# Kernel optimization log

Hardware: AMD Instinct MI355X
Metric: run time of the kernel (lower is better)

## Reference

```python
import jax, jax.numpy as jnp
import numpy as np

N_NODES = 100000
N_EDGES = 1600000
D_IN = 128
D_MSG = 128
D_HID = 128
D_EDGE = 5
D_CAT = D_IN + D_MSG  # 256
D_U1, D_U2, D_OUT = 214, 172, 128  # delta = (256-128)//3 = 42


def _leaky(x):
    return jax.nn.leaky_relu(x, negative_slope=0.01)


def setup_inputs() -> dict:
    key = jax.random.key(0)
    ks = jax.random.split(key, 12)
    def kaiming(k, shape):
        fan_in = shape[1]
        gain = np.sqrt(2.0 / (1.0 + 0.01 ** 2))
        return jax.random.normal(k, shape, dtype=jnp.float32) * (gain / np.sqrt(fan_in))
    x = jax.random.normal(ks[0], (N_NODES, D_IN), dtype=jnp.float32)
    edge_index = jax.random.randint(ks[1], (2, N_EDGES), 0, N_NODES, dtype=jnp.int64)
    edge_attr = jax.random.normal(ks[2], (N_EDGES, D_EDGE), dtype=jnp.float32)
    return {
        "x": x, "edge_index": edge_index, "edge_attr": edge_attr,
        "Wm1": kaiming(ks[3], (D_HID, D_EDGE)), "bm1": jnp.zeros((D_HID,), jnp.float32),
        "Wm2": kaiming(ks[4], (D_HID, D_HID)), "bm2": jnp.zeros((D_HID,), jnp.float32),
        "Wm3": kaiming(ks[5], (D_MSG, D_HID)), "bm3": jnp.zeros((D_MSG,), jnp.float32),
        "ln_g": jnp.ones((D_CAT,), jnp.float32), "ln_b": jnp.zeros((D_CAT,), jnp.float32),
        "Wu1": kaiming(ks[6], (D_U1, D_CAT)), "bu1": jnp.zeros((D_U1,), jnp.float32),
        "Wu2": kaiming(ks[7], (D_U2, D_U1)), "bu2": jnp.zeros((D_U2,), jnp.float32),
        "Wu3": kaiming(ks[8], (D_OUT, D_U2)), "bu3": jnp.zeros((D_OUT,), jnp.float32),
    }


def reference(x, edge_index, edge_attr, Wm1, bm1, Wm2, bm2, Wm3, bm3,
              ln_g, ln_b, Wu1, bu1, Wu2, bu2, Wu3, bu3):
    # --- message: MLP2 on edge_attr only ---  [E, D_MSG]
    h = _leaky(edge_attr @ Wm1.T + bm1)
    h = _leaky(h @ Wm2.T + bm2)
    msg = h @ Wm3.T + bm3
    # --- aggregate: scatter-add per destination node (edge_index[1]) ---
    dst = edge_index[1]
    aggr = jax.ops.segment_sum(msg, dst, num_segments=x.shape[0])  # [N, D_MSG]
    # --- update: LayerNorm(concat) then shrinking MLP ---
    cat = jnp.concatenate([x, aggr], axis=-1)  # [N, 256]
    mu = jnp.mean(cat, axis=-1, keepdims=True)
    var = jnp.mean((cat - mu) ** 2, axis=-1, keepdims=True)
    nrm = (cat - mu) * jax.lax.rsqrt(var + 1e-5) * ln_g + ln_b
    u = _leaky(nrm @ Wu1.T + bu1)
    u = _leaky(u @ Wu2.T + bu2)
    return u @ Wu3.T + bu3  # [N, D_OUT]
```

## Files before the change

### kernel.cpp

```cpp
#include <hip/hip_runtime.h>

#define N_NODES 100000
#define N_EDGES 1600000
#define STRN 264
#define NBLK_SCAN 391

#define MSG_SCALE 4096.0f
#define MSG_INV   0.000244140625f

typedef __attribute__((ext_vector_type(4))) float floatx4;
typedef __attribute__((ext_vector_type(8))) __bf16 bf16x8;
typedef __attribute__((ext_vector_type(8))) unsigned short ushort8;
typedef __attribute__((ext_vector_type(4))) unsigned short ushort4v;

#define WS_AGGR   0ull
#define WS_COUNTS 51200000ull
#define WS_OFFS   51600384ull
#define WS_PART   52000768ull
#define WS_DSTS   52002816ull
#define WS_ATTRS  58402816ull
#define WS_W2     90402816ull
#define WS_W3     (WS_W2 + 32768ull)
#define WS_WU1    (WS_W3 + 32768ull)
#define WS_WU2    (WS_WU1 + 114688ull)
#define WS_WU3    (WS_WU2 + 86016ull)
#define WS_W1     (WS_WU3 + 49152ull)

__device__ __forceinline__ unsigned short tobf(float f) {
  return __builtin_bit_cast(unsigned short, (__bf16)f);
}

__device__ __forceinline__ float leaky(float v) { return fmaxf(v, 0.01f * v); }

__device__ __forceinline__ int swz(int row, int ch) {
  return row * 128 + (ch ^ ((row & 7) << 3));
}

__device__ __forceinline__ int msw(int e, int ch) {
  return e * 16 + (ch ^ (((e >> 1) & 3) << 2));
}

__device__ __forceinline__ int dsw(int e) { return e + ((e >> 5) << 3); }

__global__ void prep_kernel(const float* __restrict__ Wm1, const float* __restrict__ Wm2,
                            const float* __restrict__ Wm3,
                            const float* __restrict__ Wu1, const float* __restrict__ Wu2,
                            const float* __restrict__ Wu3,
                            unsigned short* __restrict__ o1b,
                            unsigned short* __restrict__ o2, unsigned short* __restrict__ o3,
                            unsigned short* __restrict__ o1p, unsigned short* __restrict__ o2p,
                            unsigned short* __restrict__ o3p) {
  int i = blockIdx.x * 256 + threadIdx.x;
  if (i < 16384) {
    o2[i] = tobf(Wm2[i]);
  } else if (i < 32768) {
    int j = i - 16384; o3[j] = tobf(Wm3[j]);
  } else if (i < 32768 + 57344) {
    int j = i - 32768; int n = j >> 8, k = j & 255;
    o1p[j] = (n < 214) ? tobf(Wu1[n * 256 + k]) : (unsigned short)0;
  } else if (i < 90112 + 43008) {
    int j = i - 90112; int n = j / 224, k = j - n * 224;
    o2p[j] = (n < 172 && k < 214) ? tobf(Wu2[n * 214 + k]) : (unsigned short)0;
  } else if (i < 133120 + 24576) {
    int j = i - 133120; int n = j / 192, k = j - n * 192;
    o3p[j] = (k < 172) ? tobf(Wu3[n * 172 + k]) : (unsigned short)0;
  } else if (i < 157696 + 4096) {
    int j = i - 157696; int n = j >> 5, k = j & 31;
    o1b[j] = (k < 5) ? tobf(Wm1[n * 5 + k]) : (unsigned short)0;
  }
}

__global__ void hist_kernel(const int* __restrict__ dst, int* __restrict__ counts,
                            int* __restrict__ rank) {
  int e = blockIdx.x * 256 + threadIdx.x;
  if (e < N_EDGES) rank[e] = atomicAdd(&counts[dst[e]], 1);
}

__global__ void scanA_kernel(const int* __restrict__ counts, int* __restrict__ offs,
                             int* __restrict__ partials) {
  __shared__ int tmp[256];
  const int t = threadIdx.x;
  const int i = blockIdx.x * 256 + t;
  int v = (i < N_NODES) ? counts[i] : 0;
  tmp[t] = v;
  __syncthreads();
  for (int off = 1; off < 256; off <<= 1) {
    int a = (t >= off) ? tmp[t - off] : 0;
    __syncthreads();
    tmp[t] += a;
    __syncthreads();
  }
  if (i < N_NODES) offs[i] = tmp[t] - v;
  if (t == 255) partials[blockIdx.x] = tmp[255];
}

__global__ void scanB_kernel(int* __restrict__ partials) {
  __shared__ int tmp[512];
  const int t = threadIdx.x;
  int v = (t < NBLK_SCAN) ? partials[t] : 0;
  tmp[t] = v;
  __syncthreads();
  for (int off = 1; off < 512; off <<= 1) {
    int a = (t >= off) ? tmp[t - off] : 0;
    __syncthreads();
    tmp[t] += a;
    __syncthreads();
  }
  if (t < NBLK_SCAN) partials[t] = tmp[t] - v;
}

__global__ void scatter_kernel(const int* __restrict__ dst, const int* __restrict__ offs,
                               const int* __restrict__ parts, const int* __restrict__ rank,
                               const float* __restrict__ attr,
                               float* __restrict__ attrS, int* __restrict__ dsts) {
  int e = blockIdx.x * 256 + threadIdx.x;
  if (e < N_EDGES) {
    int d = dst[e];
    int p = offs[d] + parts[d >> 8] + rank[e];
    dsts[p] = d;
    const float* a = attr + (size_t)e * 5;
    float a0 = a[0], a1 = a[1], a2 = a[2], a3 = a[3], a4 = a[4];
    float* o = attrS + (size_t)p * 5;
    o[0] = a0; o[1] = a1; o[2] = a2; o[3] = a3; o[4] = a4;
  }
}

__global__ __launch_bounds__(256, 4) void edge_kernel(
    const float* __restrict__ attrS, const int* __restrict__ dsts,
    const unsigned short* __restrict__ W1bf, const float* __restrict__ bm1,
    const unsigned short* __restrict__ W2bf, const float* __restrict__ bm2,
    const unsigned short* __restrict__ W3bf, const float* __restrict__ bm3,
    int* __restrict__ aggr) {
  __shared__ __align__(16) char smem[33920];
  unsigned short* sH = (unsigned short*)(void*)smem;
  unsigned short* sAttrB = sH;
  int* sMsgI = (int*)(void*)smem;
  int* sDst = (int*)(void*)(smem + 33280);

  const int t = threadIdx.x;
  const int wave = t >> 6, lane = t & 63;
  const int col = lane & 15, q = lane >> 4;
  const int wbase = wave * 32;
  const long blockEdge = (long)blockIdx.x * 128;

  {
    const int e = t >> 1, half = t & 1;
    ushort8 z;
#pragma unroll
    for (int j = 0; j < 8; j++) z[j] = 0;
    if (half == 0) {
      const float* ar = attrS + (blockEdge + e) * 5;
      ushort8 v = z;
      v[0] = tobf(ar[0]); v[1] = tobf(ar[1]); v[2] = tobf(ar[2]);
      v[3] = tobf(ar[3]); v[4] = tobf(ar[4]);
      *(ushort8*)(void*)&sAttrB[e * 40] = v;
      *(ushort8*)(void*)&sAttrB[e * 40 + 8] = z;
    } else {
      *(ushort8*)(void*)&sAttrB[e * 40 + 16] = z;
      *(ushort8*)(void*)&sAttrB[e * 40 + 24] = z;
    }
    if (t < 128) sDst[dsw(t)] = dsts[blockEdge + t];
  }
  __syncthreads();

  floatx4 acc[2][8];

  {
    bf16x8 w1f[2];
#pragma unroll
    for (int i = 0; i < 2; i++)
      w1f[i] = *(const bf16x8*)(const void*)&W1bf[(wbase + i * 16 + col) * 32 + q * 8];
#pragma unroll
    for (int i = 0; i < 2; i++)
#pragma unroll
      for (int j = 0; j < 8; j++) acc[i][j] = (floatx4){0.f, 0.f, 0.f, 0.f};
#pragma unroll
    for (int et = 0; et < 8; et++) {
      bf16x8 b = *(const bf16x8*)(const void*)&sAttrB[(et * 16 + col) * 40 + q * 8];
      acc[0][et] = __builtin_amdgcn_mfma_f32_16x16x32_bf16(w1f[0], b, acc[0][et], 0, 0, 0);
      acc[1][et] = __builtin_amdgcn_mfma_f32_16x16x32_bf16(w1f[1], b, acc[1][et], 0, 0, 0);
    }
  }
  __syncthreads();

  {
    float4 blo = *(const float4*)&bm1[wbase + q * 4];
    float4 bhi = *(const float4*)&bm1[wbase + 16 + q * 4];
#pragma unroll
    for (int et = 0; et < 8; et++) {
      const int e = et * 16 + col;
      ushort4v plo, phi;
#pragma unroll
      for (int r = 0; r < 4; r++) {
        plo[r] = tobf(leaky(acc[0][et][r] + ((const float*)&blo)[r]));
        phi[r] = tobf(leaky(acc[1][et][r] + ((const float*)&bhi)[r]));
      }
      *(ushort4v*)(void*)&sH[swz(e, wbase + q * 4)] = plo;
      *(ushort4v*)(void*)&sH[swz(e, wbase + 16 + q * 4)] = phi;
    }
  }
  __syncthreads();

  {
    bf16x8 w2f[2][4];
#pragma unroll
    for (int i = 0; i < 2; i++)
#pragma unroll
      for (int ks = 0; ks < 4; ks++)
        w2f[i][ks] = *(const bf16x8*)(const void*)
            &W2bf[(wbase + i * 16 + col) * 128 + ks * 32 + q * 8];
#pragma unroll
    for (int i = 0; i < 2; i++)
#pragma unroll
      for (int j = 0; j < 8; j++) acc[i][j] = (floatx4){0.f, 0.f, 0.f, 0.f};
#pragma unroll
    for (int ks = 0; ks < 4; ks++) {
      const int kk = ks * 32 + q * 8;
#pragma unroll
      for (int et = 0; et < 8; et++) {
        bf16x8 hb = *(const bf16x8*)(const void*)&sH[swz(et * 16 + col, kk)];
        acc[0][et] = __builtin_amdgcn_mfma_f32_16x16x32_bf16(w2f[0][ks], hb, acc[0][et], 0, 0, 0);
        acc[1][et] = __builtin_amdgcn_mfma_f32_16x16x32_bf16(w2f[1][ks], hb, acc[1][et], 0, 0, 0);
      }
    }
  }
  __syncthreads();

  {
    float4 blo = *(const float4*)&bm2[wbase + q * 4];
    float4 bhi = *(const float4*)&bm2[wbase + 16 + q * 4];
#pragma unroll
    for (int et = 0; et < 8; et++) {
      const int e = et * 16 + col;
      ushort4v plo, phi;
#pragma unroll
      for (int r = 0; r < 4; r++) {
        plo[r] = tobf(leaky(acc[0][et][r] + ((const float*)&blo)[r]));
        phi[r] = tobf(leaky(acc[1][et][r] + ((const float*)&bhi)[r]));
      }
      *(ushort4v*)(void*)&sH[swz(e, wbase + q * 4)] = plo;
      *(ushort4v*)(void*)&sH[swz(e, wbase + 16 + q * 4)] = phi;
    }
  }
  __syncthreads();

  {
    bf16x8 w3f[2][4];
#pragma unroll
    for (int i = 0; i < 2; i++)
#pragma unroll
      for (int ks = 0; ks < 4; ks++)
        w3f[i][ks] = *(const bf16x8*)(const void*)
            &W3bf[(wbase + i * 16 + col) * 128 + ks * 32 + q * 8];
#pragma unroll
    for (int i = 0; i < 2; i++)
#pragma unroll
      for (int j = 0; j < 8; j++) acc[i][j] = (floatx4){0.f, 0.f, 0.f, 0.f};
#pragma unroll
    for (int ks = 0; ks < 4; ks++) {
      const int kk = ks * 32 + q * 8;
#pragma unroll
      for (int et = 0; et < 8; et++) {
        bf16x8 hb = *(const bf16x8*)(const void*)&sH[swz(et * 16 + col, kk)];
        acc[0][et] = __builtin_amdgcn_mfma_f32_16x16x32_bf16(w3f[0][ks], hb, acc[0][et], 0, 0, 0);
        acc[1][et] = __builtin_amdgcn_mfma_f32_16x16x32_bf16(w3f[1][ks], hb, acc[1][et], 0, 0, 0);
      }
    }
  }
  __syncthreads();

  const int wslab = wave * 2080;
#pragma unroll
  for (int c = 0; c < 2; c++) {
    float4 b3 = *(const float4*)&bm3[wbase + c * 16 + q * 4];
#pragma unroll
    for (int et = 0; et < 8; et++) {
      const int e = et * 16 + col;
      int4 p;
      p.x = __float2int_rn((acc[c][et][0] + b3.x) * MSG_SCALE);
      p.y = __float2int_rn((acc[c][et][1] + b3.y) * MSG_SCALE);
      p.z = __float2int_rn((acc[c][et][2] + b3.z) * MSG_SCALE);
      p.w = __float2int_rn((acc[c][et][3] + b3.w) * MSG_SCALE);
      *(int4*)(void*)&sMsgI[wslab + (et >> 1) * 8 + msw(e, q * 4)] = p;
    }
    asm volatile("s_waitcnt lgkmcnt(0)" ::: "memory");

    const int ch = col;
    const int chG = wbase + c * 16 + ch;
    const int e0 = q * 32;
    const int wbW = wslab + q * 8;
    int accv = 0;
    int dprev = sDst[dsw(e0)];
#pragma unroll 8
    for (int it = 0; it < 32; it++) {
      const int e = e0 + it;
      int d = sDst[dsw(e)];
      int iv = sMsgI[wbW + msw(e, ch)];
      if (d != dprev) {
        atomicAdd(&aggr[(size_t)dprev * 128 + chG], accv);
        accv = 0;
        dprev = d;
      }
      accv += iv;
    }
    atomicAdd(&aggr[(size_t)dprev * 128 + chG], accv);
  }
}

template <int TILES, int CT, int KST, bool FINAL>
__device__ __forceinline__ void layer_node_sw(unsigned short* __restrict__ sX,
                                              const unsigned short* __restrict__ W,
                                              const float* __restrict__ bias, int biasLim,
                                              int wave, int lane, int nodeGBase,
                                              float* __restrict__ out) {
  const int col = lane & 15, q = lane >> 4;
  const int K = KST * 32;
  floatx4 acc[CT][4];
#pragma unroll
  for (int c = 0; c < CT; c++)
#pragma unroll
    for (int n = 0; n < 4; n++) acc[c][n] = (floatx4){0.f, 0.f, 0.f, 0.f};

#pragma unroll
  for (int ks = 0; ks < KST; ks++) {
    const int kk = ks * 32 + q * 8;
    bf16x8 a[CT];
#pragma unroll
    for (int c = 0; c < CT; c++) {
      const int tile = wave + 4 * c;
      const int tc = (tile < TILES) ? tile : 0;
      a[c] = *(const bf16x8*)(const void*)&W[(tc * 16 + col) * K + kk];
    }
    bf16x8 b[4];
#pragma unroll
    for (int n = 0; n < 4; n++)
      b[n] = *(const bf16x8*)(const void*)&sX[(n * 16 + col) * STRN + kk];
#pragma unroll
    for (int c = 0; c < CT; c++) {
      if (wave + 4 * c < TILES) {
#pragma unroll
        for (int n = 0; n < 4; n++)
          acc[c][n] = __builtin_amdgcn_mfma_f32_16x16x32_bf16(a[c], b[n], acc[c][n], 0, 0, 0);
      }
    }
  }
  __syncthreads();

#pragma unroll
  for (int c = 0; c < CT; c++) {
    const int tile = wave + 4 * c;
    if (tile < TILES) {
      float bv[4];
#pragma unroll
      for (int r = 0; r < 4; r++) {
        const int ch = tile * 16 + q * 4 + r;
        bv[r] = (ch < biasLim) ? bias[ch] : 0.f;
      }
#pragma unroll
      for (int n = 0; n < 4; n++) {
        const int node = n * 16 + col;
        if (!FINAL) {
          ushort4v p;
#pragma unroll
          for (int r = 0; r < 4; r++) p[r] = tobf(leaky(acc[c][n][r] + bv[r]));
          *(ushort4v*)(void*)&sX[node * STRN + tile * 16 + q * 4] = p;
        } else {
          const long ng = (long)nodeGBase + node;
          if (ng < N_NODES) {
            float4 p = make_float4(acc[c][n][0] + bv[0], acc[c][n][1] + bv[1],
                                   acc[c][n][2] + bv[2], acc[c][n][3] + bv[3]);
            *(float4*)(void*)&out[ng * 128 + tile * 16 + q * 4] = p;
          }
        }
      }
    }
  }
  if (!FINAL) __syncthreads();
}

__global__ __launch_bounds__(256, 4) void node_kernel(
    const float* __restrict__ x, const int* __restrict__ aggr,
    const float* __restrict__ lng, const float* __restrict__ lnb,
    const unsigned short* __restrict__ Wu1p, const float* __restrict__ bu1,
    const unsigned short* __restrict__ Wu2p, const float* __restrict__ bu2,
    const unsigned short* __restrict__ Wu3p, const float* __restrict__ bu3,
    float* __restrict__ out) {
  __shared__ unsigned short sX[64 * STRN];
  __shared__ float sG[256], sB[256];
  const int t = threadIdx.x;
  const int wave = t >> 6, lane = t & 63;
  sG[t] = lng[t];
  sB[t] = lnb[t];

  const int nl = t >> 2;
  const int part = t & 3;
  const long nodeG = (long)blockIdx.x * 64 + nl;
  const bool valid = nodeG < N_NODES;
  const float* srcF = x + nodeG * 128 + part * 64;
  const int* srcI = aggr + nodeG * 128 + (part - 2) * 64;
  float s = 0.f, ss = 0.f;
  if (valid) {
#pragma unroll
    for (int i = 0; i < 16; i++) {
      float4 a;
      if (part < 2) {
        a = *(const float4*)(srcF + i * 4);
      } else {
        int4 iv = *(const int4*)(srcI + i * 4);
        a = make_float4(iv.x * MSG_INV, iv.y * MSG_INV, iv.z * MSG_INV, iv.w * MSG_INV);
      }
      s += a.x + a.y + a.z + a.w;
      ss += a.x * a.x + a.y * a.y + a.z * a.z + a.w * a.w;
    }
  }
  s += __shfl_xor(s, 1); s += __shfl_xor(s, 2);
  ss += __shfl_xor(ss, 1); ss += __shfl_xor(ss, 2);
  const float mean = s * (1.f / 256.f);
  const float var = ss * (1.f / 256.f) - mean * mean;
  const float rstd = rsqrtf(var + 1e-5f);
  __syncthreads();
  if (valid) {
    const int cb = part * 64;
#pragma unroll
    for (int i = 0; i < 16; i++) {
      float4 a;
      if (part < 2) {
        a = *(const float4*)(srcF + i * 4);
      } else {
        int4 iv = *(const int4*)(srcI + i * 4);
        a = make_float4(iv.x * MSG_INV, iv.y * MSG_INV, iv.z * MSG_INV, iv.w * MSG_INV);
      }
      int c = cb + i * 4;
      ushort4v p;
      p[0] = tobf((a.x - mean) * rstd * sG[c + 0] + sB[c + 0]);
      p[1] = tobf((a.y - mean) * rstd * sG[c + 1] + sB[c + 1]);
      p[2] = tobf((a.z - mean) * rstd * sG[c + 2] + sB[c + 2]);
      p[3] = tobf((a.w - mean) * rstd * sG[c + 3] + sB[c + 3]);
      *(ushort4v*)(void*)&sX[nl * STRN + c] = p;
    }
  }
  __syncthreads();

  const int nodeGBase = blockIdx.x * 64;
  layer_node_sw<14, 4, 8, false>(sX, Wu1p, bu1, 214, wave, lane, nodeGBase, nullptr);
  layer_node_sw<12, 3, 7, false>(sX, Wu2p, bu2, 172, wave, lane, nodeGBase, nullptr);
  layer_node_sw<8, 2, 6, true>(sX, Wu3p, bu3, 128, wave, lane, nodeGBase, out);
}

extern "C" void kernel_launch(void* const* d_in, const int* in_sizes, int n_in,
                              void* d_out, int out_size, void* d_ws, size_t ws_size,
                              hipStream_t stream) {
  const float* x    = (const float*)d_in[0];
  const int*   eidx = (const int*)d_in[1];
  const float* attr = (const float*)d_in[2];
  const float* Wm1  = (const float*)d_in[3];
  const float* bm1  = (const float*)d_in[4];
  const float* Wm2  = (const float*)d_in[5];
  const float* bm2  = (const float*)d_in[6];
  const float* Wm3  = (const float*)d_in[7];
  const float* bm3  = (const float*)d_in[8];
  const float* lng  = (const float*)d_in[9];
  const float* lnb  = (const float*)d_in[10];
  const float* Wu1  = (const float*)d_in[11];
  const float* bu1  = (const float*)d_in[12];
  const float* Wu2  = (const float*)d_in[13];
  const float* bu2  = (const float*)d_in[14];
  const float* Wu3  = (const float*)d_in[15];
  const float* bu3  = (const float*)d_in[16];
  float* out = (float*)d_out;

  char* ws = (char*)d_ws;
  int* aggr    = (int*)(ws + WS_AGGR);
  int* rank    = (int*)(ws + WS_AGGR);
  int* counts  = (int*)(ws + WS_COUNTS);
  int* offs    = (int*)(ws + WS_OFFS);
  int* parts   = (int*)(ws + WS_PART);
  int* dsts    = (int*)(ws + WS_DSTS);
  float* attrS = (float*)(ws + WS_ATTRS);
  unsigned short* W2bf = (unsigned short*)(ws + WS_W2);
  unsigned short* W3bf = (unsigned short*)(ws + WS_W3);
  unsigned short* Wu1p = (unsigned short*)(ws + WS_WU1);
  unsigned short* Wu2p = (unsigned short*)(ws + WS_WU2);
  unsigned short* Wu3p = (unsigned short*)(ws + WS_WU3);
  unsigned short* W1bf = (unsigned short*)(ws + WS_W1);

  const int* dst = eidx + N_EDGES;

  hipMemsetAsync(counts, 0, 400384, stream);
  hist_kernel<<<6250, 256, 0, stream>>>(dst, counts, rank);
  scanA_kernel<<<NBLK_SCAN, 256, 0, stream>>>(counts, offs, parts);
  scanB_kernel<<<1, 512, 0, stream>>>(parts);
  scatter_kernel<<<6250, 256, 0, stream>>>(dst, offs, parts, rank, attr, attrS, dsts);

  hipMemsetAsync(aggr, 0, (size_t)N_NODES * 128 * sizeof(int), stream);
  prep_kernel<<<632, 256, 0, stream>>>(Wm1, Wm2, Wm3, Wu1, Wu2, Wu3,
                                       W1bf, W2bf, W3bf, Wu1p, Wu2p, Wu3p);

  edge_kernel<<<N_EDGES / 128, 256, 0, stream>>>(attrS, dsts, W1bf, bm1, W2bf, bm2, W3bf,
                                                 bm3, aggr);
  node_kernel<<<(N_NODES + 63) / 64, 256, 0, stream>>>(x, aggr, lng, lnb, Wu1p, bu1, Wu2p, bu2,
                                                       Wu3p, bu3, out);
}
```

Baseline: 634.6 us.

## Pre-pack edge attrs as bf16 in scatter and remap segmented atomic reduction lanes

The scatter kernel now converts edge attributes to bf16 and writes them as padded 16-byte rows, so the edge kernel loads each row with one vector load instead of five strided float loads plus conversion. The edge kernel's reduction is also restructured. Message tiles for 64 channels are staged block-wide in shared memory in two passes, and each wave walks 32 consecutive edges with one lane per channel, reading destinations via readlane. This is meant to make the atomicAdds hit 64 contiguous ints per node row and to remove per-iteration LDS destination reads, at the cost of extra block barriers.

```diff
diff --git a/kernel.cpp b/kernel.cpp
--- a/kernel.cpp
+++ b/kernel.cpp
@@ -35,12 +35,6 @@
 __device__ __forceinline__ int swz(int row, int ch) {
   return row * 128 + (ch ^ ((row & 7) << 3));
 }
-
-__device__ __forceinline__ int msw(int e, int ch) {
-  return e * 16 + (ch ^ (((e >> 1) & 3) << 2));
-}
-
-__device__ __forceinline__ int dsw(int e) { return e + ((e >> 5) << 3); }
 
 __global__ void prep_kernel(const float* __restrict__ Wm1, const float* __restrict__ Wm2,
                             const float* __restrict__ Wm3,
@@ -112,30 +106,32 @@
 __global__ void scatter_kernel(const int* __restrict__ dst, const int* __restrict__ offs,
                                const int* __restrict__ parts, const int* __restrict__ rank,
                                const float* __restrict__ attr,
-                               float* __restrict__ attrS, int* __restrict__ dsts) {
+                               unsigned short* __restrict__ attrB, int* __restrict__ dsts) {
   int e = blockIdx.x * 256 + threadIdx.x;
   if (e < N_EDGES) {
     int d = dst[e];
     int p = offs[d] + parts[d >> 8] + rank[e];
     dsts[p] = d;
     const float* a = attr + (size_t)e * 5;
-    float a0 = a[0], a1 = a[1], a2 = a[2], a3 = a[3], a4 = a[4];
-    float* o = attrS + (size_t)p * 5;
-    o[0] = a0; o[1] = a1; o[2] = a2; o[3] = a3; o[4] = a4;
+    ushort8 v;
+    v[0] = tobf(a[0]); v[1] = tobf(a[1]); v[2] = tobf(a[2]);
+    v[3] = tobf(a[3]); v[4] = tobf(a[4]);
+    v[5] = 0; v[6] = 0; v[7] = 0;
+    *(ushort8*)(void*)&attrB[(size_t)p * 8] = v;
   }
 }
 
 __global__ __launch_bounds__(256, 4) void edge_kernel(
-    const float* __restrict__ attrS, const int* __restrict__ dsts,
+    const unsigned short* __restrict__ attrB, const int* __restrict__ dsts,
     const unsigned short* __restrict__ W1bf, const float* __restrict__ bm1,
     const unsigned short* __restrict__ W2bf, const float* __restrict__ bm2,
     const unsigned short* __restrict__ W3bf, const float* __restrict__ bm3,
     int* __restrict__ aggr) {
-  __shared__ __align__(16) char smem[33920];
+  __shared__ __align__(16) char smem[33280];
   unsigned short* sH = (unsigned short*)(void*)smem;
   unsigned short* sAttrB = sH;
   int* sMsgI = (int*)(void*)smem;
-  int* sDst = (int*)(void*)(smem + 33280);
+  int* sDst = (int*)(void*)(smem + 32768);
 
   const int t = threadIdx.x;
   const int wave = t >> 6, lane = t & 63;
@@ -143,23 +139,21 @@
   const int wbase = wave * 32;
   const long blockEdge = (long)blockIdx.x * 128;
 
+  if (t < 128) {
+    *(ushort8*)(void*)&sAttrB[t * 40] =
+        *(const ushort8*)(const void*)&attrB[(blockEdge + t) * 8];
+    sDst[t] = dsts[blockEdge + t];
+  }
   {
-    const int e = t >> 1, half = t & 1;
     ushort8 z;
 #pragma unroll
     for (int j = 0; j < 8; j++) z[j] = 0;
-    if (half == 0) {
-      const float* ar = attrS + (blockEdge + e) * 5;
-      ushort8 v = z;
-      v[0] = tobf(ar[0]); v[1] = tobf(ar[1]); v[2] = tobf(ar[2]);
-      v[3] = tobf(ar[3]); v[4] = tobf(ar[4]);
-      *(ushort8*)(void*)&sAttrB[e * 40] = v;
-      *(ushort8*)(void*)&sAttrB[e * 40 + 8] = z;
-    } else {
-      *(ushort8*)(void*)&sAttrB[e * 40 + 16] = z;
-      *(ushort8*)(void*)&sAttrB[e * 40 + 24] = z;
-    }
-    if (t < 128) sDst[dsw(t)] = dsts[blockEdge + t];
+#pragma unroll
+    for (int i = 0; i < 2; i++) {
+      const int idx = i * 256 + t;
+      const int row = idx >> 2, part = idx & 3;
+      *(ushort8*)(void*)&sAttrB[row * 40 + 8 + part * 8] = z;
+    }
   }
   __syncthreads();
 
@@ -269,33 +263,38 @@
   }
   __syncthreads();
 
-  const int wslab = wave * 2080;
+  const int dmy = sDst[wave * 32 + (lane & 31)];
+
 #pragma unroll
   for (int c = 0; c < 2; c++) {
-    float4 b3 = *(const float4*)&bm3[wbase + c * 16 + q * 4];
-#pragma unroll
-    for (int et = 0; et < 8; et++) {
-      const int e = et * 16 + col;
-      int4 p;
-      p.x = __float2int_rn((acc[c][et][0] + b3.x) * MSG_SCALE);
-      p.y = __float2int_rn((acc[c][et][1] + b3.y) * MSG_SCALE);
-      p.z = __float2int_rn((acc[c][et][2] + b3.z) * MSG_SCALE);
-      p.w = __float2int_rn((acc[c][et][3] + b3.w) * MSG_SCALE);
-      *(int4*)(void*)&sMsgI[wslab + (et >> 1) * 8 + msw(e, q * 4)] = p;
-    }
-    asm volatile("s_waitcnt lgkmcnt(0)" ::: "memory");
-
-    const int ch = col;
-    const int chG = wbase + c * 16 + ch;
-    const int e0 = q * 32;
-    const int wbW = wslab + q * 8;
+    if ((wave >> 1) == c) {
+#pragma unroll
+      for (int ci = 0; ci < 2; ci++) {
+        float4 b3 = *(const float4*)&bm3[wbase + ci * 16 + q * 4];
+        const int cb = (wbase + ci * 16 + q * 4) & 63;
+#pragma unroll
+        for (int et = 0; et < 8; et++) {
+          const int e = et * 16 + col;
+          int4 p;
+          p.x = __float2int_rn((acc[ci][et][0] + b3.x) * MSG_SCALE);
+          p.y = __float2int_rn((acc[ci][et][1] + b3.y) * MSG_SCALE);
+          p.z = __float2int_rn((acc[ci][et][2] + b3.z) * MSG_SCALE);
+          p.w = __float2int_rn((acc[ci][et][3] + b3.w) * MSG_SCALE);
+          *(int4*)(void*)&sMsgI[e * 64 + (cb ^ ((e & 7) << 2))] = p;
+        }
+      }
+    }
+    __syncthreads();
+
+    const int e0 = wave * 32;
+    const size_t chG = (size_t)c * 64 + lane;
     int accv = 0;
-    int dprev = sDst[dsw(e0)];
+    int dprev = __builtin_amdgcn_readlane(dmy, 0);
 #pragma unroll 8
     for (int it = 0; it < 32; it++) {
       const int e = e0 + it;
-      int d = sDst[dsw(e)];
-      int iv = sMsgI[wbW + msw(e, ch)];
+      const int d = __builtin_amdgcn_readlane(dmy, it);
+      const int iv = sMsgI[e * 64 + (lane ^ ((e & 7) << 2))];
       if (d != dprev) {
         atomicAdd(&aggr[(size_t)dprev * 128 + chG], accv);
         accv = 0;
@@ -304,6 +303,7 @@
       accv += iv;
     }
     atomicAdd(&aggr[(size_t)dprev * 128 + chG], accv);
+    if (c == 0) __syncthreads();
   }
 }
 
@@ -476,7 +476,7 @@
   int* offs    = (int*)(ws + WS_OFFS);
   int* parts   = (int*)(ws + WS_PART);
   int* dsts    = (int*)(ws + WS_DSTS);
-  float* attrS = (float*)(ws + WS_ATTRS);
+  unsigned short* attrB = (unsigned short*)(ws + WS_ATTRS);
   unsigned short* W2bf = (unsigned short*)(ws + WS_W2);
   unsigned short* W3bf = (unsigned short*)(ws + WS_W3);
   unsigned short* Wu1p = (unsigned short*)(ws + WS_WU1);
@@ -490,13 +490,13 @@
   hist_kernel<<<6250, 256, 0, stream>>>(dst, counts, rank);
   scanA_kernel<<<NBLK_SCAN, 256, 0, stream>>>(counts, offs, parts);
   scanB_kernel<<<1, 512, 0, stream>>>(parts);
-  scatter_kernel<<<6250, 256, 0, stream>>>(dst, offs, parts, rank, attr, attrS, dsts);
+  scatter_kernel<<<6250, 256, 0, stream>>>(dst, offs, parts, rank, attr, attrB, dsts);
 
   hipMemsetAsync(aggr, 0, (size_t)N_NODES * 128 * sizeof(int), stream);
   prep_kernel<<<632, 256, 0, stream>>>(Wm1, Wm2, Wm3, Wu1, Wu2, Wu3,
                                        W1bf, W2bf, W3bf, Wu1p, Wu2p, Wu3p);
 
-  edge_kernel<<<N_EDGES / 128, 256, 0, stream>>>(attrS, dsts, W1bf, bm1, W2bf, bm2, W3bf,
+  edge_kernel<<<N_EDGES / 128, 256, 0, stream>>>(attrB, dsts, W1bf, bm1, W2bf, bm2, W3bf,
                                                  bm3, aggr);
   node_kernel<<<(N_NODES + 63) / 64, 256, 0, stream>>>(x, aggr, lng, lnb, Wu1p, bu1, Wu2p, bu2,
                                                        Wu3p, bu3, out);
```

Measured after the change: 594.1 us. -6.4%, faster.
